# Optimization experiments

Hardware: AMD Instinct MI355X
Metric: run time of the kernel (lower is better)

The kernel has to match this reference:

```python
import jax, jax.numpy as jnp
import numpy as np

D, K, STRIDE, PADDING = 5, 3, 1, 2
B, CIN, COUT, H, W = 32, 128, 256, 56, 56


def _conv(x, w, stride, padding):
    return jax.lax.conv_general_dilated(
        x, w, window_strides=(stride, stride),
        padding=[(padding, padding), (padding, padding)],
        dimension_numbers=("NCHW", "OIHW", "NCHW"))


def setup_inputs() -> dict:
    key = jax.random.key(0)
    k1, k2, k3 = jax.random.split(key, 3)
    x = jax.random.normal(k1, (B, CIN, H, W), dtype=jnp.float32)
    # kaiming-uniform-ish core init
    fan_in = CIN * K * K
    bound = float(np.sqrt(6.0 / fan_in))
    core = jax.random.uniform(k2, (COUT, CIN, K, K), dtype=jnp.float32,
                              minval=-bound, maxval=bound)
    periphery = jax.random.uniform(k3, (D * D - K * K,), dtype=jnp.float32,
                                   minval=-0.1, maxval=0.1)
    thresh = jnp.ones((COUT,), jnp.float32) * 0.1
    scale = jnp.array([10.0], jnp.float32)
    return {"x": x, "core": core, "periphery": periphery,
            "thresh": thresh, "scale": scale}


def reference(x, core, periphery, thresh, scale):
    pad = (D - K) // 2  # offset of the KxK core inside the DxD window
    # Dense core conv: embed KxK core at the center of a DxD kernel so core
    # and periphery share the same output grid (padding=PADDING for DxD).
    core_full = jnp.pad(core, ((0, 0), (0, 0), (pad, pad), (pad, pad)))
    core_out = _conv(x, core_full, STRIDE, PADDING)  # [B, COUT, Ho, Wo]

    # Periphery: one shared scalar per off-core offset, shared across all
    # in/out channels -> sum input over channels, conv with a 1x1-channel
    # DxD stencil whose core region is zero.
    periph_mask = np.ones((D, D), dtype=bool)
    periph_mask[pad:pad + K, pad:pad + K] = False
    periph_idx = np.flatnonzero(periph_mask)  # row-major off-core offsets
    pk = jnp.zeros((D * D,), x.dtype).at[periph_idx].set(periphery)
    pk = pk.reshape(1, 1, D, D)
    xs = jnp.sum(x, axis=1, keepdims=True)  # [B,1,H,W]
    periph_out = _conv(xs, pk, STRIDE, PADDING)  # [B,1,Ho,Wo]

    # Per-out-channel threshold/scale gating: periphery term is switched on
    # where the core response exceeds the channel threshold (soft gate).
    gate = jax.nn.sigmoid(scale[0] * (core_out - thresh[None, :, None, None]))
    return core_out + gate * periph_out
```

## Files before the change

kernel.cpp:

```cpp
#include <hip/hip_runtime.h>

typedef __attribute__((__ext_vector_type__(8))) _Float16 f16x8;
typedef __attribute__((__ext_vector_type__(4))) float f32x4;
typedef __attribute__((__ext_vector_type__(4))) int i32x4;

#define HW 56
#define HW2 3136
#define CIN 128
#define COUT 256
#define NB 32
#define NPIX 100352
#define PH 58

static __device__ __forceinline__ unsigned short f2h(float f) {
  _Float16 h = (_Float16)f;
  return __builtin_bit_cast(unsigned short, h);
}

#define GLD_LDS16(g, l)                                          \
  __builtin_amdgcn_global_load_lds(                              \
      (const __attribute__((address_space(1))) void*)(g),        \
      (__attribute__((address_space(3))) void*)(l), 16, 0, 0)

__global__ __launch_bounds__(256) void zero_halo(unsigned short* __restrict__ xp) {
  int t = blockIdx.x * 256 + threadIdx.x;
  int ck = t & 15;
  int pi = t >> 4;
  int b = pi / 228, r = pi - b * 228;
  int h, w;
  if (r < 58) { h = 0; w = r; }
  else if (r < 116) { h = 57; w = r - 58; }
  else { int q = r - 116; h = 1 + (q >> 1); w = (q & 1) * 57; }
  size_t off = (((size_t)(b * PH + h) * PH + w) << 8) + (ck << 4);
  *reinterpret_cast<i32x4*>((char*)xp + off) = (i32x4){0, 0, 0, 0};
}

__global__ __launch_bounds__(256) void prep_x(const float* __restrict__ x,
                                              unsigned short* __restrict__ xp,
                                              float* __restrict__ xs) {
  __shared__ float tile[CIN * 57];
  const int bh = blockIdx.x;
  const float* src = x + (size_t)(bh / HW) * CIN * HW2 + (size_t)(bh % HW) * HW;
  for (int idx = threadIdx.x; idx < CIN * HW; idx += 256) {
    int c = idx / HW, w = idx - c * HW;
    tile[c * 57 + w] = src[(size_t)c * HW2 + w];
  }
  __syncthreads();
  unsigned short* dst =
      xp + (((size_t)(bh / HW) * PH + (bh % HW) + 1) * PH + 1) * CIN;
  for (int idx = threadIdx.x; idx < HW * (CIN / 2); idx += 256) {
    int w = idx >> 6;
    int c = (idx & 63) << 1;
    unsigned lo = f2h(tile[c * 57 + w]);
    unsigned hi = f2h(tile[(c + 1) * 57 + w]);
    *reinterpret_cast<unsigned*>(&dst[w * CIN + c]) = lo | (hi << 16);
  }
  if (threadIdx.x < HW) {
    float s = 0.f;
    for (int c = 0; c < CIN; ++c) s += tile[c * 57 + threadIdx.x];
    xs[(size_t)bh * HW + threadIdx.x] = s;
  }
}

__global__ __launch_bounds__(256) void prep_w(const float* __restrict__ core,
                                              unsigned short* __restrict__ w_t) {
  int i = blockIdx.x * 256 + threadIdx.x;
  int c = i & 127;
  int p = (i >> 7) % 9;
  int m = i / (9 * 128);
  w_t[i] = f2h(core[(size_t)(m * CIN + c) * 9 + p]);
}

__global__ __launch_bounds__(256) void periph_k(const float* __restrict__ xs,
                                                const float* __restrict__ per,
                                                float* __restrict__ po) {
  int n = blockIdx.x * 256 + threadIdx.x;
  int b = n / HW2, r = n - b * HW2;
  int ho = r / HW, wo = r - ho * HW;
  const float* xb = xs + (size_t)b * HW2;
  const int pdy[16] = {0,0,0,0,0,1,1,2,2,3,3,4,4,4,4,4};
  const int pdx[16] = {0,1,2,3,4,0,4,0,4,0,4,0,1,2,3,4};
  float acc = 0.f;
#pragma unroll
  for (int t = 0; t < 16; ++t) {
    int h = ho + pdy[t] - 2, w = wo + pdx[t] - 2;
    if ((unsigned)h < HW && (unsigned)w < HW) acc += per[t] * xb[h * HW + w];
  }
  po[n] = acc;
}

__global__ __launch_bounds__(512, 4) void gemm_k(const unsigned short* __restrict__ xp,
                                                 const unsigned short* __restrict__ w_t,
                                                 const float* __restrict__ po,
                                                 const float* __restrict__ thresh,
                                                 const float* __restrict__ scale,
                                                 float* __restrict__ out) {
  __shared__ __align__(16) char sMem[2 * 24576];

  const int tid = threadIdx.x;
  const int lane = tid & 63;
  const int wid = tid >> 6;
  const int wm = wid >> 1;
  const int wn = wid & 1;

  const int bid = blockIdx.x;
  const int n0 = ((bid & 7) * 98 + (bid >> 3)) << 7;

  const int l4 = lane >> 2;
  const int ls = lane & 3;
  const char* xpc = (const char*)xp;
  const char* wtc = (const char*)w_t;
  int aSrc[2];
#pragma unroll
  for (int k = 0; k < 2; ++k) {
    int r = wid * 32 + k * 16 + l4;
    aSrc[k] = r * 2304 + ((ls ^ ((r >> 1) & 3)) << 4);
  }
  const int aDst0 = wid * 2048;
  int bSrc;
  {
    int r = wid * 16 + l4;
    int n = n0 + r;
    int b = n / HW2, rr = n - b * HW2;
    int h = rr / HW, w = rr - h * HW;
    bSrc = ((b * PH + h + 1) * PH + (w + 1)) * 256 + ((ls ^ ((r >> 1) & 3)) << 4);
  }
  const int bDst = 16384 + wid * 1024;

  int aro[4], bro[4];
#pragma unroll
  for (int i = 0; i < 4; ++i) {
    int rowA = wm * 64 + i * 16 + (lane & 15);
    aro[i] = rowA * 64 + ((((lane >> 4) ^ (rowA >> 1)) & 3) << 4);
  }
#pragma unroll
  for (int j = 0; j < 4; ++j) {
    int rowB = wn * 64 + j * 16 + (lane & 15);
    bro[j] = 16384 + rowB * 64 + ((((lane >> 4) ^ (rowB >> 1)) & 3) << 4);
  }

  auto STAGE = [&](int buf, int t) {
    const int p = t >> 2;
    const int cq = t & 3;
    const int dy = p / 3 - 1, dx = p - (p / 3) * 3 - 1;
    const int offA = (p << 8) + (cq << 6);
    const int offB = ((dy * PH + dx) << 8) + (cq << 6);
    char* base = sMem + buf * 24576;
    GLD_LDS16(wtc + aSrc[0] + offA, base + aDst0);
    GLD_LDS16(wtc + aSrc[1] + offA, base + aDst0 + 1024);
    GLD_LDS16(xpc + bSrc + offB, base + bDst);
  };

  f32x4 acc[4][4] = {};

  STAGE(0, 0);
  __syncthreads();

  for (int t = 0; t < 36; ++t) {
    const char* base = sMem + (t & 1) * 24576;
    __builtin_amdgcn_s_barrier();
    if (t < 35) {
      STAGE((t + 1) & 1, t + 1);
      asm volatile("s_waitcnt vmcnt(3)" ::: "memory");
    } else {
      asm volatile("s_waitcnt vmcnt(0)" ::: "memory");
    }
    __builtin_amdgcn_s_barrier();

    f16x8 bfr[4];
#pragma unroll
    for (int j = 0; j < 4; ++j)
      bfr[j] = *reinterpret_cast<const f16x8*>(base + bro[j]);
#pragma unroll
    for (int i = 0; i < 4; ++i) {
      f16x8 af = *reinterpret_cast<const f16x8*>(base + aro[i]);
      __builtin_amdgcn_s_setprio(1);
#pragma unroll
      for (int j = 0; j < 4; ++j)
        acc[i][j] = __builtin_amdgcn_mfma_f32_16x16x32_f16(af, bfr[j], acc[i][j], 0, 0, 0);
      __builtin_amdgcn_s_setprio(0);
    }
  }

  const float sc = scale[0];
#pragma unroll
  for (int j = 0; j < 4; ++j) {
    int n = n0 + wn * 64 + j * 16 + (lane & 15);
    int b = n / HW2;
    int r = n - b * HW2;
    float pv = po[n];
    float* op = out + (size_t)b * (COUT * HW2) + r;
#pragma unroll
    for (int i = 0; i < 4; ++i) {
      int cl = wm * 64 + i * 16 + ((lane >> 4) << 2);
      f32x4 th = *reinterpret_cast<const f32x4*>(&thresh[cl]);
#pragma unroll
      for (int q = 0; q < 4; ++q) {
        float cv = acc[i][j][q];
        float g = 1.f / (1.f + __expf(-sc * (cv - th[q])));
        op[(size_t)(cl + q) * HW2] = cv + g * pv;
      }
    }
  }
}

extern "C" void kernel_launch(void* const* d_in, const int* in_sizes, int n_in,
                              void* d_out, int out_size, void* d_ws, size_t ws_size,
                              hipStream_t stream) {
  (void)in_sizes; (void)n_in; (void)out_size; (void)ws_size;
  const float* x      = (const float*)d_in[0];
  const float* core   = (const float*)d_in[1];
  const float* per    = (const float*)d_in[2];
  const float* thresh = (const float*)d_in[3];
  const float* scale  = (const float*)d_in[4];
  float* out = (float*)d_out;

  char* ws = (char*)d_ws;
  unsigned short* xp  = (unsigned short*)ws;
  unsigned short* w_t = (unsigned short*)(ws + 27557888);
  float* xs           = (float*)(ws + 28147712);
  float* po           = (float*)(ws + 28549120);

  zero_halo<<<(NB * 228 * 16) / 256, 256, 0, stream>>>(xp);
  prep_x<<<NB * HW, 256, 0, stream>>>(x, xp, xs);
  prep_w<<<(COUT * 9 * CIN) / 256, 256, 0, stream>>>(core, w_t);
  periph_k<<<NPIX / 256, 256, 0, stream>>>(xs, per, po);
  gemm_k<<<NPIX / 128, 512, 0, stream>>>(xp, w_t, po, thresh, scale, out);
}
```

Measured before the change: 124.3 us.

## Halve GEMM block to 4 waves with 128x64 per-wave tiles; fuse halo zeroing

The implicit-GEMM kernel now runs 256 threads (4 waves) per block instead of 8. Each wave computes a 128x64 output tile with 8x4 MFMA accumulators, and each thread issues four A and two B async global-to-LDS loads per stage. The vmcnt wait is adjusted to match. Larger per-wave tiles improve LDS fragment reuse and reduce the number of barriers per unit of work, at the cost of higher register pressure (launch bounds lowered to 256,3) and fewer waves to hide latency. The separate halo-zeroing kernel is also folded into extra blocks of prep_x, which removes one launch.

```diff
diff --git a/kernel.cpp b/kernel.cpp
--- a/kernel.cpp
+++ b/kernel.cpp
@@ -22,22 +22,22 @@
       (const __attribute__((address_space(1))) void*)(g),        \
       (__attribute__((address_space(3))) void*)(l), 16, 0, 0)
 
-__global__ __launch_bounds__(256) void zero_halo(unsigned short* __restrict__ xp) {
-  int t = blockIdx.x * 256 + threadIdx.x;
-  int ck = t & 15;
-  int pi = t >> 4;
-  int b = pi / 228, r = pi - b * 228;
-  int h, w;
-  if (r < 58) { h = 0; w = r; }
-  else if (r < 116) { h = 57; w = r - 58; }
-  else { int q = r - 116; h = 1 + (q >> 1); w = (q & 1) * 57; }
-  size_t off = (((size_t)(b * PH + h) * PH + w) << 8) + (ck << 4);
-  *reinterpret_cast<i32x4*>((char*)xp + off) = (i32x4){0, 0, 0, 0};
-}
-
 __global__ __launch_bounds__(256) void prep_x(const float* __restrict__ x,
                                               unsigned short* __restrict__ xp,
                                               float* __restrict__ xs) {
+  if (blockIdx.x >= NB * HW) {
+    int t = (blockIdx.x - NB * HW) * 256 + threadIdx.x;
+    int ck = t & 15;
+    int pi = t >> 4;
+    int b = pi / 228, r = pi - b * 228;
+    int h, w;
+    if (r < 58) { h = 0; w = r; }
+    else if (r < 116) { h = 57; w = r - 58; }
+    else { int q = r - 116; h = 1 + (q >> 1); w = (q & 1) * 57; }
+    size_t off = (((size_t)(b * PH + h) * PH + w) << 8) + (ck << 4);
+    *reinterpret_cast<i32x4*>((char*)xp + off) = (i32x4){0, 0, 0, 0};
+    return;
+  }
   __shared__ float tile[CIN * 57];
   const int bh = blockIdx.x;
   const float* src = x + (size_t)(bh / HW) * CIN * HW2 + (size_t)(bh % HW) * HW;
@@ -89,7 +89,7 @@
   po[n] = acc;
 }
 
-__global__ __launch_bounds__(512, 4) void gemm_k(const unsigned short* __restrict__ xp,
+__global__ __launch_bounds__(256, 3) void gemm_k(const unsigned short* __restrict__ xp,
                                                  const unsigned short* __restrict__ w_t,
                                                  const float* __restrict__ po,
                                                  const float* __restrict__ thresh,
@@ -108,36 +108,23 @@
 
   const int l4 = lane >> 2;
   const int ls = lane & 3;
+  const int sw = (ls ^ ((l4 >> 1) & 3)) << 4;
   const char* xpc = (const char*)xp;
   const char* wtc = (const char*)w_t;
-  int aSrc[2];
+  const int aSrc0 = (wid * 16 + l4) * 2304 + sw;
+  int bSrc[2];
 #pragma unroll
   for (int k = 0; k < 2; ++k) {
-    int r = wid * 32 + k * 16 + l4;
-    aSrc[k] = r * 2304 + ((ls ^ ((r >> 1) & 3)) << 4);
-  }
-  const int aDst0 = wid * 2048;
-  int bSrc;
-  {
-    int r = wid * 16 + l4;
-    int n = n0 + r;
+    int n = n0 + wid * 16 + k * 64 + l4;
     int b = n / HW2, rr = n - b * HW2;
     int h = rr / HW, w = rr - h * HW;
-    bSrc = ((b * PH + h + 1) * PH + (w + 1)) * 256 + ((ls ^ ((r >> 1) & 3)) << 4);
-  }
-  const int bDst = 16384 + wid * 1024;
-
-  int aro[4], bro[4];
-#pragma unroll
-  for (int i = 0; i < 4; ++i) {
-    int rowA = wm * 64 + i * 16 + (lane & 15);
-    aro[i] = rowA * 64 + ((((lane >> 4) ^ (rowA >> 1)) & 3) << 4);
-  }
-#pragma unroll
-  for (int j = 0; j < 4; ++j) {
-    int rowB = wn * 64 + j * 16 + (lane & 15);
-    bro[j] = 16384 + rowB * 64 + ((((lane >> 4) ^ (rowB >> 1)) & 3) << 4);
-  }
+    bSrc[k] = ((b * PH + h + 1) * PH + (w + 1)) * 256 + sw;
+  }
+
+  const int rowA0 = wm * 128 + (lane & 15);
+  const int aro0 = rowA0 * 64 + ((((lane >> 4) ^ (rowA0 >> 1)) & 3) << 4);
+  const int rowB0 = wn * 64 + (lane & 15);
+  const int bro0 = 16384 + rowB0 * 64 + ((((lane >> 4) ^ (rowB0 >> 1)) & 3) << 4);
 
   auto STAGE = [&](int buf, int t) {
     const int p = t >> 2;
@@ -146,12 +133,15 @@
     const int offA = (p << 8) + (cq << 6);
     const int offB = ((dy * PH + dx) << 8) + (cq << 6);
     char* base = sMem + buf * 24576;
-    GLD_LDS16(wtc + aSrc[0] + offA, base + aDst0);
-    GLD_LDS16(wtc + aSrc[1] + offA, base + aDst0 + 1024);
-    GLD_LDS16(xpc + bSrc + offB, base + bDst);
+#pragma unroll
+    for (int k = 0; k < 4; ++k)
+      GLD_LDS16(wtc + aSrc0 + k * 147456 + offA, base + (wid + 4 * k) * 1024);
+#pragma unroll
+    for (int k = 0; k < 2; ++k)
+      GLD_LDS16(xpc + bSrc[k] + offB, base + 16384 + (wid + 4 * k) * 1024);
   };
 
-  f32x4 acc[4][4] = {};
+  f32x4 acc[8][4] = {};
 
   STAGE(0, 0);
   __syncthreads();
@@ -161,7 +151,7 @@
     __builtin_amdgcn_s_barrier();
     if (t < 35) {
       STAGE((t + 1) & 1, t + 1);
-      asm volatile("s_waitcnt vmcnt(3)" ::: "memory");
+      asm volatile("s_waitcnt vmcnt(6)" ::: "memory");
     } else {
       asm volatile("s_waitcnt vmcnt(0)" ::: "memory");
     }
@@ -170,10 +160,10 @@
     f16x8 bfr[4];
 #pragma unroll
     for (int j = 0; j < 4; ++j)
-      bfr[j] = *reinterpret_cast<const f16x8*>(base + bro[j]);
-#pragma unroll
-    for (int i = 0; i < 4; ++i) {
-      f16x8 af = *reinterpret_cast<const f16x8*>(base + aro[i]);
+      bfr[j] = *reinterpret_cast<const f16x8*>(base + bro0 + j * 1024);
+#pragma unroll
+    for (int i = 0; i < 8; ++i) {
+      f16x8 af = *reinterpret_cast<const f16x8*>(base + aro0 + i * 1024);
       __builtin_amdgcn_s_setprio(1);
 #pragma unroll
       for (int j = 0; j < 4; ++j)
@@ -191,8 +181,8 @@
     float pv = po[n];
     float* op = out + (size_t)b * (COUT * HW2) + r;
 #pragma unroll
-    for (int i = 0; i < 4; ++i) {
-      int cl = wm * 64 + i * 16 + ((lane >> 4) << 2);
+    for (int i = 0; i < 8; ++i) {
+      int cl = wm * 128 + i * 16 + ((lane >> 4) << 2);
       f32x4 th = *reinterpret_cast<const f32x4*>(&thresh[cl]);
 #pragma unroll
       for (int q = 0; q < 4; ++q) {
@@ -221,9 +211,8 @@
   float* xs           = (float*)(ws + 28147712);
   float* po           = (float*)(ws + 28549120);
 
-  zero_halo<<<(NB * 228 * 16) / 256, 256, 0, stream>>>(xp);
-  prep_x<<<NB * HW, 256, 0, stream>>>(x, xp, xs);
+  prep_x<<<NB * HW + 456, 256, 0, stream>>>(x, xp, xs);
   prep_w<<<(COUT * 9 * CIN) / 256, 256, 0, stream>>>(core, w_t);
   periph_k<<<NPIX / 256, 256, 0, stream>>>(xs, per, po);
-  gemm_k<<<NPIX / 128, 512, 0, stream>>>(xp, w_t, po, thresh, scale, out);
-}
+  gemm_k<<<NPIX / 128, 256, 0, stream>>>(xp, w_t, po, thresh, scale, out);
+}
```

New measurement: 120.8 us. -2.8%, faster.

## Fuse halo zeroing and periphery stencil into other kernels; triple-buffer GEMM

Applied to the files above, without the earlier changes.

Folds the halo-zeroing kernel into extra blocks of prep_x and computes the periphery stencil inside the GEMM epilogue, which removes two launches and the po round trip. The GEMM pipeline moves from double to triple buffering with a prefetch depth of two, and launch bounds drop to 2 waves per SIMD so it can afford the larger LDS footprint. The swizzle term is simplified using the fact that the row parity pattern equals l4. Risks are lower occupancy and 16 extra scattered loads per output column in the epilogue.

```diff
diff --git a/kernel.cpp b/kernel.cpp
--- a/kernel.cpp
+++ b/kernel.cpp
@@ -22,22 +22,22 @@
       (const __attribute__((address_space(1))) void*)(g),        \
       (__attribute__((address_space(3))) void*)(l), 16, 0, 0)
 
-__global__ __launch_bounds__(256) void zero_halo(unsigned short* __restrict__ xp) {
-  int t = blockIdx.x * 256 + threadIdx.x;
-  int ck = t & 15;
-  int pi = t >> 4;
-  int b = pi / 228, r = pi - b * 228;
-  int h, w;
-  if (r < 58) { h = 0; w = r; }
-  else if (r < 116) { h = 57; w = r - 58; }
-  else { int q = r - 116; h = 1 + (q >> 1); w = (q & 1) * 57; }
-  size_t off = (((size_t)(b * PH + h) * PH + w) << 8) + (ck << 4);
-  *reinterpret_cast<i32x4*>((char*)xp + off) = (i32x4){0, 0, 0, 0};
-}
-
 __global__ __launch_bounds__(256) void prep_x(const float* __restrict__ x,
                                               unsigned short* __restrict__ xp,
                                               float* __restrict__ xs) {
+  if (blockIdx.x >= NB * HW) {
+    int t = (blockIdx.x - NB * HW) * 256 + threadIdx.x;
+    int ck = t & 15;
+    int pi = t >> 4;
+    int b = pi / 228, r = pi - b * 228;
+    int h, w;
+    if (r < 58) { h = 0; w = r; }
+    else if (r < 116) { h = 57; w = r - 58; }
+    else { int q = r - 116; h = 1 + (q >> 1); w = (q & 1) * 57; }
+    size_t off = (((size_t)(b * PH + h) * PH + w) << 8) + (ck << 4);
+    *reinterpret_cast<i32x4*>((char*)xp + off) = (i32x4){0, 0, 0, 0};
+    return;
+  }
   __shared__ float tile[CIN * 57];
   const int bh = blockIdx.x;
   const float* src = x + (size_t)(bh / HW) * CIN * HW2 + (size_t)(bh % HW) * HW;
@@ -71,31 +71,14 @@
   w_t[i] = f2h(core[(size_t)(m * CIN + c) * 9 + p]);
 }
 
-__global__ __launch_bounds__(256) void periph_k(const float* __restrict__ xs,
-                                                const float* __restrict__ per,
-                                                float* __restrict__ po) {
-  int n = blockIdx.x * 256 + threadIdx.x;
-  int b = n / HW2, r = n - b * HW2;
-  int ho = r / HW, wo = r - ho * HW;
-  const float* xb = xs + (size_t)b * HW2;
-  const int pdy[16] = {0,0,0,0,0,1,1,2,2,3,3,4,4,4,4,4};
-  const int pdx[16] = {0,1,2,3,4,0,4,0,4,0,4,0,1,2,3,4};
-  float acc = 0.f;
-#pragma unroll
-  for (int t = 0; t < 16; ++t) {
-    int h = ho + pdy[t] - 2, w = wo + pdx[t] - 2;
-    if ((unsigned)h < HW && (unsigned)w < HW) acc += per[t] * xb[h * HW + w];
-  }
-  po[n] = acc;
-}
-
-__global__ __launch_bounds__(512, 4) void gemm_k(const unsigned short* __restrict__ xp,
+__global__ __launch_bounds__(512, 2) void gemm_k(const unsigned short* __restrict__ xp,
                                                  const unsigned short* __restrict__ w_t,
-                                                 const float* __restrict__ po,
+                                                 const float* __restrict__ xs,
+                                                 const float* __restrict__ per,
                                                  const float* __restrict__ thresh,
                                                  const float* __restrict__ scale,
                                                  float* __restrict__ out) {
-  __shared__ __align__(16) char sMem[2 * 24576];
+  __shared__ __align__(16) char sMem[3 * 24576];
 
   const int tid = threadIdx.x;
   const int lane = tid & 63;
@@ -108,13 +91,14 @@
 
   const int l4 = lane >> 2;
   const int ls = lane & 3;
+  const int sw = (ls ^ ((l4 >> 1) & 3)) << 4;
   const char* xpc = (const char*)xp;
   const char* wtc = (const char*)w_t;
   int aSrc[2];
 #pragma unroll
   for (int k = 0; k < 2; ++k) {
     int r = wid * 32 + k * 16 + l4;
-    aSrc[k] = r * 2304 + ((ls ^ ((r >> 1) & 3)) << 4);
+    aSrc[k] = r * 2304 + sw;
   }
   const int aDst0 = wid * 2048;
   int bSrc;
@@ -123,7 +107,7 @@
     int n = n0 + r;
     int b = n / HW2, rr = n - b * HW2;
     int h = rr / HW, w = rr - h * HW;
-    bSrc = ((b * PH + h + 1) * PH + (w + 1)) * 256 + ((ls ^ ((r >> 1) & 3)) << 4);
+    bSrc = ((b * PH + h + 1) * PH + (w + 1)) * 256 + sw;
   }
   const int bDst = 16384 + wid * 1024;
 
@@ -154,13 +138,16 @@
   f32x4 acc[4][4] = {};
 
   STAGE(0, 0);
-  __syncthreads();
-
+  STAGE(1, 1);
+
+  int cb = 0, sb = 2;
   for (int t = 0; t < 36; ++t) {
-    const char* base = sMem + (t & 1) * 24576;
+    const char* base = sMem + cb * 24576;
     __builtin_amdgcn_s_barrier();
-    if (t < 35) {
-      STAGE((t + 1) & 1, t + 1);
+    if (t < 34) {
+      STAGE(sb, t + 2);
+      asm volatile("s_waitcnt vmcnt(6)" ::: "memory");
+    } else if (t == 34) {
       asm volatile("s_waitcnt vmcnt(3)" ::: "memory");
     } else {
       asm volatile("s_waitcnt vmcnt(0)" ::: "memory");
@@ -180,15 +167,26 @@
         acc[i][j] = __builtin_amdgcn_mfma_f32_16x16x32_f16(af, bfr[j], acc[i][j], 0, 0, 0);
       __builtin_amdgcn_s_setprio(0);
     }
+    cb = (cb == 2) ? 0 : cb + 1;
+    sb = (sb == 2) ? 0 : sb + 1;
   }
 
   const float sc = scale[0];
+  static const int pdy[16] = {0,0,0,0,0,1,1,2,2,3,3,4,4,4,4,4};
+  static const int pdx[16] = {0,1,2,3,4,0,4,0,4,0,4,0,1,2,3,4};
 #pragma unroll
   for (int j = 0; j < 4; ++j) {
     int n = n0 + wn * 64 + j * 16 + (lane & 15);
     int b = n / HW2;
     int r = n - b * HW2;
-    float pv = po[n];
+    int ho = r / HW, wo = r - ho * HW;
+    const float* xb = xs + (size_t)b * HW2;
+    float pv = 0.f;
+#pragma unroll
+    for (int tt = 0; tt < 16; ++tt) {
+      int h = ho + pdy[tt] - 2, w = wo + pdx[tt] - 2;
+      if ((unsigned)h < HW && (unsigned)w < HW) pv += per[tt] * xb[h * HW + w];
+    }
     float* op = out + (size_t)b * (COUT * HW2) + r;
 #pragma unroll
     for (int i = 0; i < 4; ++i) {
@@ -219,11 +217,8 @@
   unsigned short* xp  = (unsigned short*)ws;
   unsigned short* w_t = (unsigned short*)(ws + 27557888);
   float* xs           = (float*)(ws + 28147712);
-  float* po           = (float*)(ws + 28549120);
-
-  zero_halo<<<(NB * 228 * 16) / 256, 256, 0, stream>>>(xp);
-  prep_x<<<NB * HW, 256, 0, stream>>>(x, xp, xs);
+
+  prep_x<<<NB * HW + 456, 256, 0, stream>>>(x, xp, xs);
   prep_w<<<(COUT * 9 * CIN) / 256, 256, 0, stream>>>(core, w_t);
-  periph_k<<<NPIX / 256, 256, 0, stream>>>(xs, per, po);
-  gemm_k<<<NPIX / 128, 512, 0, stream>>>(xp, w_t, po, thresh, scale, out);
-}
+  gemm_k<<<NPIX / 128, 512, 0, stream>>>(xp, w_t, xs, per, thresh, scale, out);
+}
```

Result: no change. 126.3 us (+1.6%).

## Split GEMM output tile into 128x128 blocks over two channel halves; fuse halo zeroing into prep_x

Applied to the files above, without the earlier changes.

The implicit-GEMM conv kernel moves from a 256x128 tile with 512 threads to a 128x128 tile with 256 threads. Each block now covers one half of the output channels, which doubles the grid and cuts LDS per block, aiming at better occupancy and load balance. Input pixels are now loaded twice, once per channel half, so global traffic for the activations goes up. The halo-zeroing kernel is folded into prep_x as extra blocks to save one launch.

```diff
diff --git a/kernel.cpp b/kernel.cpp
--- a/kernel.cpp
+++ b/kernel.cpp
@@ -22,22 +22,22 @@
       (const __attribute__((address_space(1))) void*)(g),        \
       (__attribute__((address_space(3))) void*)(l), 16, 0, 0)
 
-__global__ __launch_bounds__(256) void zero_halo(unsigned short* __restrict__ xp) {
-  int t = blockIdx.x * 256 + threadIdx.x;
-  int ck = t & 15;
-  int pi = t >> 4;
-  int b = pi / 228, r = pi - b * 228;
-  int h, w;
-  if (r < 58) { h = 0; w = r; }
-  else if (r < 116) { h = 57; w = r - 58; }
-  else { int q = r - 116; h = 1 + (q >> 1); w = (q & 1) * 57; }
-  size_t off = (((size_t)(b * PH + h) * PH + w) << 8) + (ck << 4);
-  *reinterpret_cast<i32x4*>((char*)xp + off) = (i32x4){0, 0, 0, 0};
-}
-
 __global__ __launch_bounds__(256) void prep_x(const float* __restrict__ x,
                                               unsigned short* __restrict__ xp,
                                               float* __restrict__ xs) {
+  if (blockIdx.x >= NB * HW) {
+    int t = (blockIdx.x - NB * HW) * 256 + threadIdx.x;
+    int ck = t & 15;
+    int pi = t >> 4;
+    int b = pi / 228, r = pi - b * 228;
+    int h, w;
+    if (r < 58) { h = 0; w = r; }
+    else if (r < 116) { h = 57; w = r - 58; }
+    else { int q = r - 116; h = 1 + (q >> 1); w = (q & 1) * 57; }
+    size_t off = (((size_t)(b * PH + h) * PH + w) << 8) + (ck << 4);
+    *reinterpret_cast<i32x4*>((char*)xp + off) = (i32x4){0, 0, 0, 0};
+    return;
+  }
   __shared__ float tile[CIN * 57];
   const int bh = blockIdx.x;
   const float* src = x + (size_t)(bh / HW) * CIN * HW2 + (size_t)(bh % HW) * HW;
@@ -89,13 +89,13 @@
   po[n] = acc;
 }
 
-__global__ __launch_bounds__(512, 4) void gemm_k(const unsigned short* __restrict__ xp,
+__global__ __launch_bounds__(256, 4) void gemm_k(const unsigned short* __restrict__ xp,
                                                  const unsigned short* __restrict__ w_t,
                                                  const float* __restrict__ po,
                                                  const float* __restrict__ thresh,
                                                  const float* __restrict__ scale,
                                                  float* __restrict__ out) {
-  __shared__ __align__(16) char sMem[2 * 24576];
+  __shared__ __align__(16) char sMem[2 * 16384];
 
   const int tid = threadIdx.x;
   const int lane = tid & 63;
@@ -104,28 +104,27 @@
   const int wn = wid & 1;
 
   const int bid = blockIdx.x;
-  const int n0 = ((bid & 7) * 98 + (bid >> 3)) << 7;
+  const int sb = (bid & 7) * 196 + (bid >> 3);
+  const int m0 = (sb & 1) << 7;
+  const int n0 = (sb >> 1) << 7;
 
   const int l4 = lane >> 2;
   const int ls = lane & 3;
+  const int sw = (ls ^ ((l4 >> 1) & 3)) << 4;
   const char* xpc = (const char*)xp;
   const char* wtc = (const char*)w_t;
-  int aSrc[2];
+  int aSrc[2], bSrc[2];
 #pragma unroll
   for (int k = 0; k < 2; ++k) {
     int r = wid * 32 + k * 16 + l4;
-    aSrc[k] = r * 2304 + ((ls ^ ((r >> 1) & 3)) << 4);
-  }
-  const int aDst0 = wid * 2048;
-  int bSrc;
-  {
-    int r = wid * 16 + l4;
+    aSrc[k] = (m0 + r) * 2304 + sw;
     int n = n0 + r;
     int b = n / HW2, rr = n - b * HW2;
     int h = rr / HW, w = rr - h * HW;
-    bSrc = ((b * PH + h + 1) * PH + (w + 1)) * 256 + ((ls ^ ((r >> 1) & 3)) << 4);
-  }
-  const int bDst = 16384 + wid * 1024;
+    bSrc[k] = ((b * PH + h + 1) * PH + (w + 1)) * 256 + sw;
+  }
+  const int aDst = wid * 2048;
+  const int bDst = 8192 + wid * 2048;
 
   int aro[4], bro[4];
 #pragma unroll
@@ -136,7 +135,7 @@
 #pragma unroll
   for (int j = 0; j < 4; ++j) {
     int rowB = wn * 64 + j * 16 + (lane & 15);
-    bro[j] = 16384 + rowB * 64 + ((((lane >> 4) ^ (rowB >> 1)) & 3) << 4);
+    bro[j] = 8192 + rowB * 64 + ((((lane >> 4) ^ (rowB >> 1)) & 3) << 4);
   }
 
   auto STAGE = [&](int buf, int t) {
@@ -145,10 +144,11 @@
     const int dy = p / 3 - 1, dx = p - (p / 3) * 3 - 1;
     const int offA = (p << 8) + (cq << 6);
     const int offB = ((dy * PH + dx) << 8) + (cq << 6);
-    char* base = sMem + buf * 24576;
-    GLD_LDS16(wtc + aSrc[0] + offA, base + aDst0);
-    GLD_LDS16(wtc + aSrc[1] + offA, base + aDst0 + 1024);
-    GLD_LDS16(xpc + bSrc + offB, base + bDst);
+    char* base = sMem + buf * 16384;
+    GLD_LDS16(wtc + aSrc[0] + offA, base + aDst);
+    GLD_LDS16(wtc + aSrc[1] + offA, base + aDst + 1024);
+    GLD_LDS16(xpc + bSrc[0] + offB, base + bDst);
+    GLD_LDS16(xpc + bSrc[1] + offB, base + bDst + 1024);
   };
 
   f32x4 acc[4][4] = {};
@@ -157,11 +157,11 @@
   __syncthreads();
 
   for (int t = 0; t < 36; ++t) {
-    const char* base = sMem + (t & 1) * 24576;
+    const char* base = sMem + (t & 1) * 16384;
     __builtin_amdgcn_s_barrier();
     if (t < 35) {
       STAGE((t + 1) & 1, t + 1);
-      asm volatile("s_waitcnt vmcnt(3)" ::: "memory");
+      asm volatile("s_waitcnt vmcnt(4)" ::: "memory");
     } else {
       asm volatile("s_waitcnt vmcnt(0)" ::: "memory");
     }
@@ -192,7 +192,7 @@
     float* op = out + (size_t)b * (COUT * HW2) + r;
 #pragma unroll
     for (int i = 0; i < 4; ++i) {
-      int cl = wm * 64 + i * 16 + ((lane >> 4) << 2);
+      int cl = m0 + wm * 64 + i * 16 + ((lane >> 4) << 2);
       f32x4 th = *reinterpret_cast<const f32x4*>(&thresh[cl]);
 #pragma unroll
       for (int q = 0; q < 4; ++q) {
@@ -221,9 +221,8 @@
   float* xs           = (float*)(ws + 28147712);
   float* po           = (float*)(ws + 28549120);
 
-  zero_halo<<<(NB * 228 * 16) / 256, 256, 0, stream>>>(xp);
-  prep_x<<<NB * HW, 256, 0, stream>>>(x, xp, xs);
+  prep_x<<<NB * HW + 456, 256, 0, stream>>>(x, xp, xs);
   prep_w<<<(COUT * 9 * CIN) / 256, 256, 0, stream>>>(core, w_t);
   periph_k<<<NPIX / 256, 256, 0, stream>>>(xs, per, po);
-  gemm_k<<<NPIX / 128, 512, 0, stream>>>(xp, w_t, po, thresh, scale, out);
-}
+  gemm_k<<<2 * (NPIX / 128), 256, 0, stream>>>(xp, w_t, po, thresh, scale, out);
+}
```

Measured after the change: 117.6 us. 5.4% less time.
